# Optimization experiments

Hardware: AMD Instinct MI355X
Metric: run time of the kernel (lower is better)

The kernel has to match this reference:

```python
import jax, jax.numpy as jnp
import numpy as np

C = 128          # num_channel
NEI = 9          # patch_size / neighbor
R = NEI // 2     # displacement radius (4)
B, H, W = 4, 200, 200


def conv2d(x, w, b, pad):
    # x: [N,C,H,W], w: [O,I,kh,kw]
    y = jax.lax.conv_general_dilated(
        x, w, window_strides=(1, 1), padding=[(pad, pad), (pad, pad)],
        dimension_numbers=('NCHW', 'OIHW', 'NCHW'))
    return y + b[None, :, None, None]


def setup_inputs() -> dict:
    key = jax.random.key(0)
    ks = jax.random.split(key, 16)
    s = 0.02
    return {
        'feature_select': jax.random.normal(ks[0], (B, C, H, W), jnp.float32),
        'feature_current': jax.random.normal(ks[1], (B, C, H, W), jnp.float32),
        # embedding convs
        'ec1_w': jax.random.normal(ks[2], (64, C, 1, 1), jnp.float32) * s,
        'ec1_b': jnp.zeros((64,), jnp.float32),
        'ec2_w': jax.random.normal(ks[3], (64, 64, 3, 3), jnp.float32) * s,
        'ec2_b': jnp.zeros((64,), jnp.float32),
        # aggregation convs
        'ag1_w': jax.random.normal(ks[4], (64, C, 1, 1), jnp.float32) * s,
        'ag1_b': jnp.zeros((64,), jnp.float32),
        'ag2_w': jax.random.normal(ks[5], (32, 64, 3, 3), jnp.float32) * s,
        'ag2_b': jnp.zeros((32,), jnp.float32),
        'ag3_w': jax.random.normal(ks[6], (1, 32, 1, 1), jnp.float32) * s,
        'ag3_b': jnp.zeros((1,), jnp.float32),
    }


def reference(feature_select, feature_current, ec1_w, ec1_b, ec2_w, ec2_b,
              ag1_w, ag1_b, ag2_w, ag2_b, ag3_w, ag3_b):
    b, c, h, w = feature_select.shape
    # --- shared embedding network ---
    cat = jnp.concatenate([feature_select, feature_current], axis=0)
    e = jax.nn.relu(conv2d(cat, ec1_w, ec1_b, 0))
    e = jax.nn.relu(conv2d(e, ec2_w, ec2_b, 1))
    e_sel, e_cur = e[:b], e[b:]   # (torch code names these current/select, order follows concat)
    # --- correlation: 9x9 patch, kernel_size=1, zero-padded displaced neighbors ---
    ep = jnp.pad(e_cur, ((0, 0), (0, 0), (R, R), (R, R)))
    corr = []
    for di in range(-R, R + 1):
        for dj in range(-R, R + 1):
            nb = ep[:, :, R + di:R + di + h, R + dj:R + dj + w]
            corr.append(jnp.sum(e_sel * nb, axis=1))  # [b,h,w]
    weights = jax.nn.softmax(jnp.stack(corr, axis=1), axis=1)  # [b,81,h,w]
    # --- neighbor-weighted feature alignment ---
    sp = jnp.pad(feature_select, ((0, 0), (0, 0), (R, R), (R, R)))
    align = jnp.zeros_like(feature_select)
    k = 0
    for di in range(-R, R + 1):
        for dj in range(-R, R + 1):
            align = align + weights[:, k:k + 1] * sp[:, :, R + di:R + di + h, R + dj:R + dj + w]
            k += 1
    # --- aggregation: adaptive 2-way blend ---
    fc = jnp.concatenate([align, feature_current], axis=0)
    a = jax.nn.relu(conv2d(fc, ag1_w, ag1_b, 0))
    a = jax.nn.relu(conv2d(a, ag2_w, ag2_b, 1))
    a = jax.nn.relu(conv2d(a, ag3_w, ag3_b, 0))  # [2b,1,h,w]
    w2 = jax.nn.softmax(jnp.concatenate([a[:b], a[b:]], axis=1), axis=1)
    return w2[:, 0:1] * align + w2[:, 1:2] * feature_current
```

## Files before the change

### kernel.cpp

```cpp
#include <hip/hip_runtime.h>

namespace {
constexpr int H = 200, W = 200, HW = H * W;
constexpr int Bz = 4;
constexpr int PW = 208, PH = 202, PPLANE = PW * PH;
constexpr int EPW = 208, EPH = 208, EPL = EPW * EPH;
}

typedef __attribute__((ext_vector_type(8))) short bf16x8;
typedef __attribute__((ext_vector_type(4))) float f32x4;

__device__ inline ushort f2bf(float f) {
  unsigned u = __float_as_uint(f);
  u += 0x7fffu + ((u >> 16) & 1u);
  return (ushort)(u >> 16);
}

__global__ __launch_bounds__(256) void zero_k(uint4* __restrict__ p, int n) {
  int i = blockIdx.x * 256 + threadIdx.x;
  if (i < n) p[i] = uint4{0u, 0u, 0u, 0u};
}

__global__ __launch_bounds__(256) void wxform_k(const float* __restrict__ w,
                                                ushort* __restrict__ wb, int cout) {
  int i = blockIdx.x * 256 + threadIdx.x;
  int tot = cout * 64 * 9;
  if (i >= tot) return;
  int co = i / (64 * 9);
  int r = i % (64 * 9);
  int ci = r / 9, tap = r % 9;
  wb[(tap * cout + co) * 64 + ci] = f2bf(w[i]);
}

template <int CIN>
__global__ __launch_bounds__(256) void conv1x1_nhwc_k(
    const float* __restrict__ srcA, const float* __restrict__ srcB,
    const float* __restrict__ w, const float* __restrict__ bias,
    ushort* __restrict__ out) {
  __shared__ float wt[CIN * 64];
  for (int i = threadIdx.x; i < CIN * 64; i += 256) {
    int ci = i >> 6, co = i & 63;
    wt[i] = w[co * CIN + ci];
  }
  __syncthreads();
  int p = blockIdx.x * 256 + threadIdx.x;
  int bb = p / HW, pix = p % HW;
  const float* src =
      (bb < Bz ? srcA + (size_t)bb * CIN * HW : srcB + (size_t)(bb - Bz) * CIN * HW) + pix;
  float acc[64];
#pragma unroll
  for (int co = 0; co < 64; co++) acc[co] = bias[co];
  for (int ci = 0; ci < CIN; ci++) {
    float x = src[(size_t)ci * HW];
    const float4* w4 = (const float4*)&wt[ci * 64];
#pragma unroll
    for (int q = 0; q < 16; q++) {
      float4 wv = w4[q];
      acc[4 * q + 0] += x * wv.x;
      acc[4 * q + 1] += x * wv.y;
      acc[4 * q + 2] += x * wv.z;
      acc[4 * q + 3] += x * wv.w;
    }
  }
  int y = pix / W, x = pix % W;
  ushort* o = out + ((size_t)bb * PPLANE + (size_t)(y + 1) * PW + (x + 1)) * 64;
  uint4* o4 = (uint4*)o;
#pragma unroll
  for (int g = 0; g < 8; g++) {
    unsigned u0 = (unsigned)f2bf(fmaxf(acc[8 * g + 0], 0.f)) |
                  ((unsigned)f2bf(fmaxf(acc[8 * g + 1], 0.f)) << 16);
    unsigned u1 = (unsigned)f2bf(fmaxf(acc[8 * g + 2], 0.f)) |
                  ((unsigned)f2bf(fmaxf(acc[8 * g + 3], 0.f)) << 16);
    unsigned u2 = (unsigned)f2bf(fmaxf(acc[8 * g + 4], 0.f)) |
                  ((unsigned)f2bf(fmaxf(acc[8 * g + 5], 0.f)) << 16);
    unsigned u3 = (unsigned)f2bf(fmaxf(acc[8 * g + 6], 0.f)) |
                  ((unsigned)f2bf(fmaxf(acc[8 * g + 7], 0.f)) << 16);
    o4[g] = uint4{u0, u1, u2, u3};
  }
}

template <int COUT, bool NHWC>
__global__ __launch_bounds__(256) void conv3x3_mfma_k(
    const ushort* __restrict__ in, const ushort* __restrict__ wb,
    const float* __restrict__ bias, float* __restrict__ outf,
    ushort* __restrict__ outh) {
  constexpr int NF = COUT / 16;
  __shared__ ushort As[272 * 72];
  __shared__ ushort Bs[3 * COUT * 64];
  const int tile = blockIdx.x, img = blockIdx.y;
  const int pp0 = PW + tile * 256;
  const int tid = threadIdx.x, wave = tid >> 6, lane = tid & 63;
  const int lm = lane & 15, lq = lane >> 4;
  const ushort* inb = in + (size_t)img * PPLANE * 64;

  f32x4 acc[4][NF];
#pragma unroll
  for (int mf = 0; mf < 4; mf++)
#pragma unroll
    for (int nf = 0; nf < NF; nf++) acc[mf][nf] = f32x4{0.f, 0.f, 0.f, 0.f};

  for (int dy = 0; dy < 3; dy++) {
    __syncthreads();
    long abase = ((long)pp0 + (long)(dy - 1) * PW - 8) * 64;
    for (int i = tid; i < 272 * 8; i += 256) {
      int m = i >> 3, kseg = i & 7;
      uint4 v = *(const uint4*)(inb + abase + (long)m * 64 + kseg * 8);
      *(uint4*)&As[m * 72 + kseg * 8] = v;
    }
    for (int i = tid; i < 3 * COUT * 8; i += 256) {
      int dx = i / (COUT * 8);
      int r = i % (COUT * 8);
      int co = r >> 3, kseg = r & 7;
      uint4 v = *(const uint4*)(wb + (((size_t)(dy * 3 + dx) * COUT + co) << 6) + kseg * 8);
      *(uint4*)&Bs[(dx * COUT + co) * 64 + ((kseg ^ (co & 7)) * 8)] = v;
    }
    __syncthreads();
#pragma unroll
    for (int dx = 0; dx < 3; dx++) {
#pragma unroll
      for (int kc = 0; kc < 2; kc++) {
        bf16x8 bfr[NF];
#pragma unroll
        for (int nf = 0; nf < NF; nf++) {
          int n = nf * 16 + lm;
          int kb = kc * 4 + lq;
          bfr[nf] = *(const bf16x8*)&Bs[(dx * COUT + n) * 64 + ((kb ^ (n & 7)) * 8)];
        }
#pragma unroll
        for (int mf = 0; mf < 4; mf++) {
          int mo = (wave * 4 + mf) * 16 + lm;
          bf16x8 afr = *(const bf16x8*)&As[(mo + dx + 7) * 72 + kc * 32 + lq * 8];
#pragma unroll
          for (int nf = 0; nf < NF; nf++)
            acc[mf][nf] = __builtin_amdgcn_mfma_f32_16x16x32_bf16(afr, bfr[nf],
                                                                  acc[mf][nf], 0, 0, 0);
        }
      }
    }
  }
  float bv[NF];
#pragma unroll
  for (int nf = 0; nf < NF; nf++) bv[nf] = bias[nf * 16 + lm];
#pragma unroll
  for (int mf = 0; mf < 4; mf++) {
#pragma unroll
    for (int nf = 0; nf < NF; nf++) {
      int co = nf * 16 + lm;
#pragma unroll
      for (int r = 0; r < 4; r++) {
        int mo = pp0 + (wave * 4 + mf) * 16 + lq * 4 + r;
        int py = mo / PW, px = mo % PW;
        if (py >= 1 && py <= H && px >= 1 && px <= W) {
          float v = fmaxf(acc[mf][nf][r] + bv[nf], 0.f);
          if (NHWC) {
            ushort* eo = outh + (size_t)img * EPL * 64;
            eo[(((size_t)(py + 3)) * EPW + (px + 3)) * 64 + co] = f2bf(v);
          } else {
            outf[((size_t)img * COUT + co) * HW + (py - 1) * W + (px - 1)] = v;
          }
        }
      }
    }
  }
}

__global__ __launch_bounds__(128) void corr_mfma_k(
    const ushort* __restrict__ e, ushort* __restrict__ wgt) {
  __shared__ float S[2 * 16 * 91];
  const int wave = threadIdx.x >> 6, lane = threadIdx.x & 63;
  const int x0 = blockIdx.x * 16;
  const int y = blockIdx.y * 2 + wave;
  const int b = blockIdx.z;
  const int nl = lane & 15, kq = lane >> 4;
  const ushort* es = e + (size_t)b * EPL * 64;
  const ushort* ec = e + (size_t)(b + 4) * EPL * 64;
  size_t abase = ((size_t)(y + 4) * EPW + (size_t)(4 + x0 + nl)) * 64 + kq * 8;
  bf16x8 afr0 = *(const bf16x8*)(es + abase);
  bf16x8 afr1 = *(const bf16x8*)(es + abase + 32);
  float* Sw = &S[wave * 16 * 91];
  for (int di = 0; di < 9; di++) {
    const ushort* erow = ec + ((size_t)(y + di) * EPW + x0) * 64;
#pragma unroll
    for (int nh = 0; nh < 2; nh++) {
      f32x4 g = f32x4{0.f, 0.f, 0.f, 0.f};
      const ushort* bp = erow + (size_t)(nh * 16 + nl) * 64 + kq * 8;
      bf16x8 b0 = *(const bf16x8*)(bp);
      bf16x8 b1 = *(const bf16x8*)(bp + 32);
      g = __builtin_amdgcn_mfma_f32_16x16x32_bf16(afr0, b0, g, 0, 0, 0);
      g = __builtin_amdgcn_mfma_f32_16x16x32_bf16(afr1, b1, g, 0, 0, 0);
      int q = nh * 16 + nl;
#pragma unroll
      for (int r = 0; r < 4; r++) {
        int m = kq * 4 + r;
        int s = q - m;
        if (s >= 0 && s <= 8) Sw[m * 91 + di * 9 + s] = g[r];
      }
    }
  }
  int px = lane >> 2, lg = lane & 3;
  float* Sp = &Sw[px * 91];
  float mx = -1e30f;
  for (int k = lg; k < 81; k += 4) mx = fmaxf(mx, Sp[k]);
  mx = fmaxf(mx, __shfl_xor(mx, 1));
  mx = fmaxf(mx, __shfl_xor(mx, 2));
  float sum = 0.f;
  for (int k = lg; k < 81; k += 4) {
    float t = expf(Sp[k] - mx);
    Sp[k] = t;
    sum += t;
  }
  sum += __shfl_xor(sum, 1);
  sum += __shfl_xor(sum, 2);
  float rinv = 1.f / sum;
  if (x0 + px < W) {
    ushort* wp = wgt + (size_t)b * 81 * HW + (size_t)y * W + x0 + px;
    for (int k = lg; k < 81; k += 4) wp[(size_t)k * HW] = f2bf(Sp[k] * rinv);
  }
}

__global__ __launch_bounds__(256, 3) void align_mfma2_k(
    const ushort* __restrict__ wgt, const float* __restrict__ fs,
    float* __restrict__ out) {
  __shared__ alignas(16) ushort As2[16 * 16 * 40];
  __shared__ alignas(16) ushort Fs2[24 * 16 * 40];
  const int tid = threadIdx.x;
  int bid = blockIdx.x;
  int p = bid & 7;
  int rank = bid >> 3;
  const int b = p >> 1, h = p & 1;
  const int cgi = rank & 3;
  int tile = rank >> 2;
  const int ty = tile / 13, tx = tile % 13;
  const int x0 = tx * 16, y0 = ty * 16;
  const int c0 = (h * 4 + cgi) * 16;

  for (int i = tid; i < 1280; i += 256) *(uint4*)&As2[i * 8] = uint4{0u, 0u, 0u, 0u};

  const int srow = tid >> 4, sm = tid & 15;
  const bool sval = (y0 + srow < H) && (x0 + sm < W);
  const ushort* wrow =
      wgt + (size_t)b * 81 * HW + (size_t)(y0 + srow) * W + (x0 + sm);
  ushort wv[9];
  if (sval) {
#pragma unroll
    for (int dj = 0; dj < 9; dj++) wv[dj] = wrow[(size_t)dj * HW];
  }

  {
    const float* fb = fs + ((size_t)b * 128 + c0) * HW;
    for (int i = tid; i < 24 * 16 * 32; i += 256) {
      int k = i & 31;
      int c = (i >> 5) & 15;
      int rf = i >> 9;
      int gy = y0 - 4 + rf, gx = x0 - 4 + k;
      float v = 0.f;
      if (k < 24 && gy >= 0 && gy < H && gx >= 0 && gx < W)
        v = fb[(size_t)c * HW + (size_t)gy * W + gx];
      Fs2[(rf * 16 + c) * 40 + k] = f2bf(v);
    }
  }
  __syncthreads();

  const int lane = tid & 63, wave = tid >> 6;
  const int nl = lane & 15, kq = lane >> 4;
  f32x4 acc[4];
#pragma unroll
  for (int rr = 0; rr < 4; rr++) acc[rr] = f32x4{0.f, 0.f, 0.f, 0.f};

  for (int di = 0; di < 9; ++di) {
    if (sval) {
#pragma unroll
      for (int dj = 0; dj < 9; dj++)
        As2[(srow * 16 + sm) * 40 + sm + dj] = wv[dj];
    }
    if (di < 8 && sval) {
      const ushort* wn = wrow + (size_t)((di + 1) * 9) * HW;
#pragma unroll
      for (int dj = 0; dj < 9; dj++) wv[dj] = wn[(size_t)dj * HW];
    }
    __syncthreads();
#pragma unroll
    for (int rr = 0; rr < 4; ++rr) {
      int row = wave * 4 + rr;
      bf16x8 af = *(const bf16x8*)&As2[(row * 16 + nl) * 40 + kq * 8];
      int rf = row + di;
      bf16x8 bf = *(const bf16x8*)&Fs2[(rf * 16 + nl) * 40 + kq * 8];
      acc[rr] = __builtin_amdgcn_mfma_f32_16x16x32_bf16(af, bf, acc[rr], 0, 0, 0);
    }
    __syncthreads();
  }

  const int xs = x0 + kq * 4;
  if (xs + 3 < W) {
    int c = c0 + nl;
#pragma unroll
    for (int rr = 0; rr < 4; ++rr) {
      int y = y0 + wave * 4 + rr;
      if (y < H) {
        *(float4*)&out[((size_t)b * 128 + c) * HW + (size_t)y * W + xs] =
            float4{acc[rr][0], acc[rr][1], acc[rr][2], acc[rr][3]};
      }
    }
  }
}

__global__ __launch_bounds__(256) void final_k(
    const float* __restrict__ a2, const float* __restrict__ w3,
    const float* __restrict__ b3, const float* __restrict__ alignb,
    const float* __restrict__ fcur, float* __restrict__ out) {
  int p = blockIdx.x * 256 + threadIdx.x;
  int bb = p / HW, pix = p % HW;
  const float* aS = a2 + (size_t)bb * 32 * HW + pix;
  const float* aC = a2 + (size_t)(bb + Bz) * 32 * HW + pix;
  float s0 = b3[0], s1 = b3[0];
#pragma unroll
  for (int c = 0; c < 32; c++) {
    float wv = w3[c];
    s0 += wv * aS[(size_t)c * HW];
    s1 += wv * aC[(size_t)c * HW];
  }
  s0 = fmaxf(s0, 0.f);
  s1 = fmaxf(s1, 0.f);
  float m = fmaxf(s0, s1);
  float e0 = expf(s0 - m), e1 = expf(s1 - m);
  float inv = 1.f / (e0 + e1);
  float p0 = e0 * inv, p1 = e1 * inv;
  const float* al = alignb + (size_t)bb * 128 * HW + pix;
  const float* fc = fcur + (size_t)bb * 128 * HW + pix;
  float* o = out + (size_t)bb * 128 * HW + pix;
#pragma unroll 4
  for (int c = 0; c < 128; c++)
    o[(size_t)c * HW] = p0 * al[(size_t)c * HW] + p1 * fc[(size_t)c * HW];
}

extern "C" void kernel_launch(void* const* d_in, const int* in_sizes, int n_in,
                              void* d_out, int out_size, void* d_ws, size_t ws_size,
                              hipStream_t stream) {
  const float* fsel = (const float*)d_in[0];
  const float* fcur = (const float*)d_in[1];
  const float* ec1_w = (const float*)d_in[2];
  const float* ec1_b = (const float*)d_in[3];
  const float* ec2_w = (const float*)d_in[4];
  const float* ec2_b = (const float*)d_in[5];
  const float* ag1_w = (const float*)d_in[6];
  const float* ag1_b = (const float*)d_in[7];
  const float* ag2_w = (const float*)d_in[8];
  const float* ag2_b = (const float*)d_in[9];
  const float* ag3_w = (const float*)d_in[10];
  const float* ag3_b = (const float*)d_in[11];

  char* ws = (char*)d_ws;
  size_t off = 4096;
  ushort* padbuf = (ushort*)(ws + off);
  size_t padbuf_bytes = (size_t)8 * PPLANE * 64 * 2;
  off += padbuf_bytes;
  ushort* epad = (ushort*)(ws + off);
  size_t epad_bytes = (size_t)8 * EPL * 64 * 2;
  off += epad_bytes + 4096;
  ushort* wgtb = (ushort*)(ws + off);
  off += (size_t)4 * 81 * HW * 2 + 4096;
  float* alignb = (float*)(ws + off);
  off += (size_t)4 * 128 * HW * 4;
  ushort* wb1 = (ushort*)(ws + off);
  off += 9 * 64 * 64 * 2;
  ushort* wb2 = (ushort*)(ws + off);
  off += 9 * 32 * 64 * 2;
  float* a2 = (float*)epad;
  float* outp = (float*)d_out;

  dim3 blk(256);
  const int MTILES = (200 * PW + 255) / 256;

  wxform_k<<<(9 * 64 * 64 + 255) / 256, blk, 0, stream>>>(ec2_w, wb1, 64);
  wxform_k<<<(9 * 32 * 64 + 255) / 256, blk, 0, stream>>>(ag2_w, wb2, 32);
  {
    int nz = (int)((padbuf_bytes + epad_bytes) / 16);
    zero_k<<<(nz + 255) / 256, blk, 0, stream>>>((uint4*)padbuf, nz);
  }
  conv1x1_nhwc_k<128><<<1250, blk, 0, stream>>>(fsel, fcur, ec1_w, ec1_b, padbuf);
  conv3x3_mfma_k<64, true><<<dim3(MTILES, 8), blk, 0, stream>>>(
      padbuf, wb1, ec2_b, nullptr, epad);
  corr_mfma_k<<<dim3(13, 100, 4), dim3(128), 0, stream>>>(epad, wgtb);
  align_mfma2_k<<<5408, blk, 0, stream>>>(wgtb, fsel, alignb);
  conv1x1_nhwc_k<128><<<1250, blk, 0, stream>>>(alignb, fcur, ag1_w, ag1_b, padbuf);
  conv3x3_mfma_k<32, false><<<dim3(MTILES, 8), blk, 0, stream>>>(
      padbuf, wb2, ag2_b, a2, nullptr);
  final_k<<<625, blk, 0, stream>>>(a2, ag3_w, ag3_b, alignb, fcur, outp);
}
```

Measured before the change: 874.5 us.

## Store softmax weights pixel-major and double-buffer align A tiles

```diff
diff --git a/kernel.cpp b/kernel.cpp
--- a/kernel.cpp
+++ b/kernel.cpp
@@ -5,6 +5,7 @@
 constexpr int Bz = 4;
 constexpr int PW = 208, PH = 202, PPLANE = PW * PH;
 constexpr int EPW = 208, EPH = 208, EPL = EPW * EPH;
+constexpr int WST = 96;
 }
 
 typedef __attribute__((ext_vector_type(8))) short bf16x8;
@@ -213,15 +214,15 @@
   sum += __shfl_xor(sum, 2);
   float rinv = 1.f / sum;
   if (x0 + px < W) {
-    ushort* wp = wgt + (size_t)b * 81 * HW + (size_t)y * W + x0 + px;
-    for (int k = lg; k < 81; k += 4) wp[(size_t)k * HW] = f2bf(Sp[k] * rinv);
-  }
-}
-
-__global__ __launch_bounds__(256, 3) void align_mfma2_k(
+    ushort* wp = wgt + ((size_t)b * 40000 + (size_t)y * W + x0 + px) * WST;
+    for (int k = lg; k < 81; k += 4) wp[(k / 9) * 10 + k % 9] = f2bf(Sp[k] * rinv);
+  }
+}
+
+__global__ __launch_bounds__(256, 2) void align_mfma3_k(
     const ushort* __restrict__ wgt, const float* __restrict__ fs,
     float* __restrict__ out) {
-  __shared__ alignas(16) ushort As2[16 * 16 * 40];
+  __shared__ alignas(16) ushort As2[2 * 16 * 16 * 40];
   __shared__ alignas(16) ushort Fs2[24 * 16 * 40];
   const int tid = threadIdx.x;
   int bid = blockIdx.x;
@@ -234,19 +235,51 @@
   const int x0 = tx * 16, y0 = ty * 16;
   const int c0 = (h * 4 + cgi) * 16;
 
-  for (int i = tid; i < 1280; i += 256) *(uint4*)&As2[i * 8] = uint4{0u, 0u, 0u, 0u};
+  for (int i = tid; i < 2560; i += 256)
+    *(uint4*)&As2[i * 8] = uint4{0u, 0u, 0u, 0u};
 
   const int srow = tid >> 4, sm = tid & 15;
   const bool sval = (y0 + srow < H) && (x0 + sm < W);
-  const ushort* wrow =
-      wgt + (size_t)b * 81 * HW + (size_t)(y0 + srow) * W + (x0 + sm);
-  ushort wv[9];
+  const ushort* wpix =
+      wgt + ((size_t)b * 40000 + (size_t)(y0 + srow) * W + (x0 + sm)) * WST;
+  uint4 wa = uint4{0u, 0u, 0u, 0u};
+  ushort w8 = 0;
   if (sval) {
-#pragma unroll
-    for (int dj = 0; dj < 9; dj++) wv[dj] = wrow[(size_t)dj * HW];
-  }
-
-  {
+    const uint* wp32 = (const uint*)wpix;
+    wa.x = wp32[0]; wa.y = wp32[1]; wa.z = wp32[2]; wa.w = wp32[3];
+    w8 = wpix[8];
+  }
+  __syncthreads();
+
+  const bool interior = (tx >= 1 && tx <= 11 && ty >= 1 && ty <= 11);
+  if (interior) {
+    const float* fb =
+        fs + ((size_t)b * 128 + c0) * HW + (size_t)(y0 - 4) * W + (x0 - 4);
+    for (int i = tid; i < 384; i += 256) {
+      int c = i & 15, rf = i >> 4;
+      const float4* src = (const float4*)(fb + (size_t)c * HW + (size_t)rf * W);
+      float4 f0 = src[0], f1 = src[1], f2 = src[2];
+      float4 f3 = src[3], f4 = src[4], f5 = src[5];
+      ushort* dst = &Fs2[(rf * 16 + c) * 40];
+      uint4 o;
+      o.x = (uint)f2bf(f0.x) | ((uint)f2bf(f0.y) << 16);
+      o.y = (uint)f2bf(f0.z) | ((uint)f2bf(f0.w) << 16);
+      o.z = (uint)f2bf(f1.x) | ((uint)f2bf(f1.y) << 16);
+      o.w = (uint)f2bf(f1.z) | ((uint)f2bf(f1.w) << 16);
+      *(uint4*)&dst[0] = o;
+      o.x = (uint)f2bf(f2.x) | ((uint)f2bf(f2.y) << 16);
+      o.y = (uint)f2bf(f2.z) | ((uint)f2bf(f2.w) << 16);
+      o.z = (uint)f2bf(f3.x) | ((uint)f2bf(f3.y) << 16);
+      o.w = (uint)f2bf(f3.z) | ((uint)f2bf(f3.w) << 16);
+      *(uint4*)&dst[8] = o;
+      o.x = (uint)f2bf(f4.x) | ((uint)f2bf(f4.y) << 16);
+      o.y = (uint)f2bf(f4.z) | ((uint)f2bf(f4.w) << 16);
+      o.z = (uint)f2bf(f5.x) | ((uint)f2bf(f5.y) << 16);
+      o.w = (uint)f2bf(f5.z) | ((uint)f2bf(f5.w) << 16);
+      *(uint4*)&dst[16] = o;
+      *(uint4*)&dst[24] = uint4{0u, 0u, 0u, 0u};
+    }
+  } else {
     const float* fb = fs + ((size_t)b * 128 + c0) * HW;
     for (int i = tid; i < 24 * 16 * 32; i += 256) {
       int k = i & 31;
@@ -259,6 +292,18 @@
       Fs2[(rf * 16 + c) * 40 + k] = f2bf(v);
     }
   }
+
+  if (sval) {
+    ushort* ap = &As2[(srow * 16 + sm) * 40 + sm];
+    ap[0] = (ushort)wa.x; ap[1] = (ushort)(wa.x >> 16);
+    ap[2] = (ushort)wa.y; ap[3] = (ushort)(wa.y >> 16);
+    ap[4] = (ushort)wa.z; ap[5] = (ushort)(wa.z >> 16);
+    ap[6] = (ushort)wa.w; ap[7] = (ushort)(wa.w >> 16);
+    ap[8] = w8;
+    const uint* wp32 = (const uint*)(wpix + 10);
+    wa.x = wp32[0]; wa.y = wp32[1]; wa.z = wp32[2]; wa.w = wp32[3];
+    w8 = wpix[18];
+  }
   __syncthreads();
 
   const int lane = tid & 63, wave = tid >> 6;
@@ -268,24 +313,28 @@
   for (int rr = 0; rr < 4; rr++) acc[rr] = f32x4{0.f, 0.f, 0.f, 0.f};
 
   for (int di = 0; di < 9; ++di) {
-    if (sval) {
-#pragma unroll
-      for (int dj = 0; dj < 9; dj++)
-        As2[(srow * 16 + sm) * 40 + sm + dj] = wv[dj];
-    }
-    if (di < 8 && sval) {
-      const ushort* wn = wrow + (size_t)((di + 1) * 9) * HW;
-#pragma unroll
-      for (int dj = 0; dj < 9; dj++) wv[dj] = wn[(size_t)dj * HW];
-    }
-    __syncthreads();
+    const ushort* Ab = &As2[(di & 1) * 10240];
 #pragma unroll
     for (int rr = 0; rr < 4; ++rr) {
       int row = wave * 4 + rr;
-      bf16x8 af = *(const bf16x8*)&As2[(row * 16 + nl) * 40 + kq * 8];
-      int rf = row + di;
-      bf16x8 bf = *(const bf16x8*)&Fs2[(rf * 16 + nl) * 40 + kq * 8];
+      bf16x8 af = *(const bf16x8*)&Ab[(row * 16 + nl) * 40 + kq * 8];
+      bf16x8 bf = *(const bf16x8*)&Fs2[((row + di) * 16 + nl) * 40 + kq * 8];
       acc[rr] = __builtin_amdgcn_mfma_f32_16x16x32_bf16(af, bf, acc[rr], 0, 0, 0);
+    }
+    if (di < 8) {
+      if (sval) {
+        ushort* ap = &As2[((di & 1) ^ 1) * 10240 + (srow * 16 + sm) * 40 + sm];
+        ap[0] = (ushort)wa.x; ap[1] = (ushort)(wa.x >> 16);
+        ap[2] = (ushort)wa.y; ap[3] = (ushort)(wa.y >> 16);
+        ap[4] = (ushort)wa.z; ap[5] = (ushort)(wa.z >> 16);
+        ap[6] = (ushort)wa.w; ap[7] = (ushort)(wa.w >> 16);
+        ap[8] = w8;
+        if (di < 7) {
+          const uint* wp32 = (const uint*)(wpix + 10 * (di + 2));
+          wa.x = wp32[0]; wa.y = wp32[1]; wa.z = wp32[2]; wa.w = wp32[3];
+          w8 = wpix[10 * (di + 2) + 8];
+        }
+      }
     }
     __syncthreads();
   }
@@ -358,7 +407,7 @@
   size_t epad_bytes = (size_t)8 * EPL * 64 * 2;
   off += epad_bytes + 4096;
   ushort* wgtb = (ushort*)(ws + off);
-  off += (size_t)4 * 81 * HW * 2 + 4096;
+  off += (size_t)4 * 40000 * WST * 2 + 4096;
   float* alignb = (float*)(ws + off);
   off += (size_t)4 * 128 * HW * 4;
   ushort* wb1 = (ushort*)(ws + off);
@@ -381,7 +430,7 @@
   conv3x3_mfma_k<64, true><<<dim3(MTILES, 8), blk, 0, stream>>>(
       padbuf, wb1, ec2_b, nullptr, epad);
   corr_mfma_k<<<dim3(13, 100, 4), dim3(128), 0, stream>>>(epad, wgtb);
-  align_mfma2_k<<<5408, blk, 0, stream>>>(wgtb, fsel, alignb);
+  align_mfma3_k<<<5408, blk, 0, stream>>>(wgtb, fsel, alignb);
   conv1x1_nhwc_k<128><<<1250, blk, 0, stream>>>(alignb, fcur, ag1_w, ag1_b, padbuf);
   conv3x3_mfma_k<32, false><<<dim3(MTILES, 8), blk, 0, stream>>>(
       padbuf, wb2, ag2_b, a2, nullptr);
```

After: 815.1 us. 1.07x faster.
